# Performance work log

Measured on AMD Instinct MI355X. Metric: run time of the kernel, lower is better.

Reference implementation:

```python
import jax, jax.numpy as jnp
import numpy as np

H = 8   # heads
C = 64  # per-head channels (gnn_hidden_dim)
HID = H * C  # 512
IN_CH = 6
EMB = 64
U, M = 16, 512
N_NODES = U * M  # 8192
N_EDGES = 131072


def _tconv(x, src, dst, Wq, bq, Wk, bk, Wv, bv, Ws, bs):
    """PyG TransformerConv (concat=True, root_weight=True, beta=False, eval mode)."""
    N = x.shape[0]
    q = (x @ Wq + bq).reshape(N, H, C)
    k = (x @ Wk + bk).reshape(N, H, C)
    v = (x @ Wv + bv).reshape(N, H, C)
    # per-edge attention scores: query at dst (target i), key at src (source j)
    score = jnp.einsum('ehc,ehc->eh', q[dst], k[src]) / jnp.sqrt(jnp.float32(C))
    # segment softmax over incoming edges of each dst node
    mx = jax.ops.segment_max(score, dst, num_segments=N)
    ex = jnp.exp(score - mx[dst])
    denom = jax.ops.segment_sum(ex, dst, num_segments=N)
    alpha = ex / (denom[dst] + 1e-16)  # [E, H]
    msg = alpha[..., None] * v[src]    # [E, H, C]
    out = jax.ops.segment_sum(msg, dst, num_segments=N).reshape(N, HID)
    return out + x @ Ws + bs  # root/skip connection


def setup_inputs() -> dict:
    key = jax.random.key(0)
    ks = iter(jax.random.split(key, 64))
    s = 0.05

    def lin(k, i, o):
        k1, k2 = jax.random.split(k)
        return (jax.random.normal(k1, (i, o), jnp.float32) * s,
                jax.random.normal(k2, (o,), jnp.float32) * s)

    inp = {}
    inp['mission_coords'] = jax.random.uniform(next(ks), (M, 2), jnp.float32)
    inp['uavs_info'] = jax.random.uniform(next(ks), (U, 2), jnp.float32)
    inp['speeds'] = jax.random.uniform(next(ks), (U,), jnp.float32)
    inp['dist_matrix'] = jax.random.uniform(next(ks), (U, M), jnp.float32)
    inp['timetogo_matrix'] = jax.random.uniform(next(ks), (U, M), jnp.float32)
    inp['action_mask'] = jax.random.randint(next(ks), (U, M), 0, 2, jnp.int32)
    inp['edge_index'] = jax.random.randint(next(ks), (2, N_EDGES), 0, N_NODES, jnp.int64)
    inp['batch'] = jnp.zeros((U,), jnp.int64)

    # layer 0 (in=6)
    inp['Wq0'], inp['bq0'] = lin(next(ks), IN_CH, HID)
    inp['Wk0'], inp['bk0'] = lin(next(ks), IN_CH, HID)
    inp['Wv0'], inp['bv0'] = lin(next(ks), IN_CH, HID)
    inp['Ws0'], inp['bs0'] = lin(next(ks), IN_CH, HID)
    # layers 1..3 stacked (in=512)
    for nm in ['Wq', 'Wk', 'Wv', 'Ws']:
        Ws_, bs_ = [], []
        for _ in range(3):
            w, b = lin(next(ks), HID, HID)
            Ws_.append(w); bs_.append(b)
        inp[nm] = jnp.stack(Ws_)
        inp['b' + nm[1:].lower()] = jnp.stack(bs_)
    inp['Wout'], inp['bout'] = lin(next(ks), HID, EMB)
    inp['Wa1'], inp['ba1'] = lin(next(ks), EMB + 3, 128)
    inp['Wa2'], inp['ba2'] = lin(next(ks), 128, 1)
    inp['Wc1'], inp['bc1'] = lin(next(ks), EMB + 3, 128)
    inp['Wc2'], inp['bc2'] = lin(next(ks), 128, 1)
    return inp


def reference(mission_coords, uavs_info, speeds, dist_matrix, timetogo_matrix,
              action_mask, edge_index, batch,
              Wq0, bq0, Wk0, bk0, Wv0, bv0, Ws0, bs0,
              Wq, bq, Wk, bk, Wv, bv, Ws, bs,
              Wout, bout, Wa1, ba1, Wa2, ba2, Wc1, bc1, Wc2, bc2):
    u, m = uavs_info.shape[0], mission_coords.shape[0]
    mc = jnp.broadcast_to(mission_coords[None], (u, m, 2))
    mask_e = action_mask[..., None].astype(jnp.float32)
    sp_e = jnp.broadcast_to(speeds[:, None, None], (u, m, 1))
    x = jnp.concatenate([mc, mask_e, sp_e, dist_matrix[..., None],
                         timetogo_matrix[..., None]], axis=-1).reshape(u * m, IN_CH)
    src, dst = edge_index[0], edge_index[1]
    x = jax.nn.relu(_tconv(x, src, dst, Wq0, bq0, Wk0, bk0, Wv0, bv0, Ws0, bs0))
    for l in range(3):
        x = jax.nn.relu(_tconv(x, src, dst, Wq[l], bq[l], Wk[l], bk[l],
                               Wv[l], bv[l], Ws[l], bs[l]))
    x = x @ Wout + bout  # [U*M, EMB]
    uav_emb = x.reshape(u, m, EMB).sum(axis=1)  # sum pooling over missions
    combined = jnp.concatenate([uavs_info, uav_emb, speeds[:, None]], axis=-1)
    logits = jax.nn.relu(combined @ Wa1 + ba1) @ Wa2 + ba2  # [U, 1]
    action_probs = jax.nn.softmax(logits, axis=-1)
    state_values = (jax.nn.relu(combined @ Wc1 + bc1) @ Wc2 + bc2).squeeze()
    return action_probs, state_values
```

## Files before the change

### kernel.cpp

```cpp
#include <hip/hip_runtime.h>
#include <hip/hip_bf16.h>
#include <math.h>

#define NNODES 8192
#define NEDGES 131072
#define HID    512
#define UU     16
#define MM     512
#define NQKVS  2048

typedef __attribute__((ext_vector_type(8))) short bf16x8;
typedef __attribute__((ext_vector_type(4))) float f32x4;

__device__ __forceinline__ float bf2f(ushort u) {
    return __uint_as_float(((unsigned)u) << 16);
}
__device__ __forceinline__ ushort f2bf(float f) {
    unsigned x = __float_as_uint(f);
    return (ushort)((x + 0x7fffu + ((x >> 16) & 1u)) >> 16);
}

__global__ __launch_bounds__(256) void k_build_x(
    const float* __restrict__ mc, const float* __restrict__ speeds,
    const float* __restrict__ dist, const float* __restrict__ ttg,
    const int* __restrict__ mask, float* __restrict__ x6)
{
    int n = blockIdx.x * blockDim.x + threadIdx.x;
    if (n >= NNODES) return;
    int u = n >> 9, m = n & 511;
    float* o = x6 + (size_t)n * 6;
    o[0] = mc[m * 2 + 0];
    o[1] = mc[m * 2 + 1];
    o[2] = (float)mask[u * MM + m];
    o[3] = speeds[u];
    o[4] = dist[u * MM + m];
    o[5] = ttg[u * MM + m];
}

__global__ __launch_bounds__(256) void k_wt(
    const float* __restrict__ Wq, const float* __restrict__ Wk,
    const float* __restrict__ Wv, const float* __restrict__ Ws,
    ushort* __restrict__ Wt)
{
    __shared__ float tile[64][65];
    int z = blockIdx.z;
    int l = z >> 2, which = z & 3;
    const float* src = (which == 0 ? Wq : which == 1 ? Wk : which == 2 ? Wv : Ws)
                       + (size_t)l * HID * HID;
    int k0 = blockIdx.x * 64, c0 = blockIdx.y * 64;
    int t = threadIdx.x;
#pragma unroll
    for (int i = 0; i < 16; ++i) {
        int idx = i * 256 + t;
        int r = idx >> 6, c = idx & 63;
        tile[r][c] = src[(size_t)(k0 + r) * HID + c0 + c];
    }
    __syncthreads();
    ushort* dst = Wt + ((size_t)l * NQKVS + which * HID + c0) * HID + k0;
#pragma unroll
    for (int i = 0; i < 16; ++i) {
        int idx = i * 256 + t;
        int r = idx >> 6, c = idx & 63;
        dst[(size_t)r * HID + c] = f2bf(tile[c][r]);
    }
}

__global__ __launch_bounds__(256) void k_bias(
    const float* __restrict__ bq, const float* __restrict__ bk,
    const float* __restrict__ bv, const float* __restrict__ bs,
    float* __restrict__ bcat)
{
    int i = blockIdx.x * 256 + threadIdx.x;
    int l = i >> 11, j = i & 2047;
    int which = j >> 9, jj = j & 511;
    const float* b = which == 0 ? bq : which == 1 ? bk : which == 2 ? bv : bs;
    bcat[i] = b[l * HID + jj];
}

__global__ __launch_bounds__(256) void k_lin0(
    const float* __restrict__ x6,
    const float* __restrict__ Wq0, const float* __restrict__ bq0,
    const float* __restrict__ Wk0, const float* __restrict__ bk0,
    const float* __restrict__ Wv0, const float* __restrict__ bv0,
    const float* __restrict__ Ws0, const float* __restrict__ bs0,
    ushort* __restrict__ Y)
{
    int n = blockIdx.x;
    int j = threadIdx.x;
    int col0 = j * 8;
    int which = col0 >> 9, jj = col0 & 511;
    const float* W = which == 0 ? Wq0 : which == 1 ? Wk0 : which == 2 ? Wv0 : Ws0;
    const float* b = which == 0 ? bq0 : which == 1 ? bk0 : which == 2 ? bv0 : bs0;
    const float* xr = x6 + (size_t)n * 6;
    float x[6];
#pragma unroll
    for (int t = 0; t < 6; ++t) x[t] = xr[t];
    float s[8];
#pragma unroll
    for (int u = 0; u < 8; ++u) s[u] = b[jj + u];
#pragma unroll
    for (int t = 0; t < 6; ++t)
#pragma unroll
        for (int u = 0; u < 8; ++u)
            s[u] = fmaf(x[t], W[t * HID + jj + u], s[u]);
    bf16x8 o8;
#pragma unroll
    for (int u = 0; u < 8; ++u) o8[u] = (short)f2bf(s[u]);
    *(bf16x8*)(Y + (size_t)n * NQKVS + col0) = o8;
}

#define GBM 128
#define GBN 128
#define GBK 64
#define TILEB (GBM * GBK * 2)
#define BUFB  (2 * TILEB)

__device__ __forceinline__ void stage_tile(
    const ushort* __restrict__ Ag, const ushort* __restrict__ Bg,
    char* __restrict__ base, int t)
{
    const int lane = t & 63;
    const int w = t >> 6;
    const int r8 = lane >> 3;
    const int c  = lane & 7;
    const int csw = c ^ r8;
#pragma unroll
    for (int i = 0; i < 4; ++i) {
        int r0 = (w * 4 + i) * 8;
        __builtin_amdgcn_global_load_lds(
            (const __attribute__((address_space(1))) void*)(Ag + (size_t)(r0 + r8) * HID + csw * 8),
            (__attribute__((address_space(3))) void*)(base + r0 * 128 + lane * 16), 16, 0, 0);
        __builtin_amdgcn_global_load_lds(
            (const __attribute__((address_space(1))) void*)(Bg + (size_t)(r0 + r8) * HID + csw * 8),
            (__attribute__((address_space(3))) void*)(base + TILEB + r0 * 128 + lane * 16), 16, 0, 0);
    }
}

__global__ __launch_bounds__(256, 2) void k_gemm(
    const ushort* __restrict__ A,
    const ushort* __restrict__ Bt,
    const float* __restrict__ bias,
    ushort* __restrict__ Y)
{
    __shared__ char lds[2 * BUFB];
    const int t = threadIdx.x;
    const int m0 = blockIdx.x * GBM, n0 = blockIdx.y * GBN;
    const int wid = t >> 6, lane = t & 63;
    const int wr = wid >> 1, wc = wid & 1;
    const int l15 = lane & 15, lkq = lane >> 4;

    f32x4 acc[4][4] = {};

    const ushort* Ab = A + (size_t)m0 * HID;
    const ushort* Bb = Bt + (size_t)n0 * HID;

    stage_tile(Ab, Bb, lds, t);
    int cur = 0;
    const int NKS = HID / GBK;
    for (int T = 0; T < NKS; ++T) {
        __syncthreads();
        if (T + 1 < NKS)
            stage_tile(Ab + (T + 1) * GBK, Bb + (T + 1) * GBK,
                       lds + (cur ^ 1) * BUFB, t);
        const char* la = lds + cur * BUFB;
        const char* lb = la + TILEB;
#pragma unroll
        for (int kh = 0; kh < 2; ++kh) {
            const int kq = kh * 4 + lkq;
            const int sw = (kq ^ (l15 & 7)) << 4;
            bf16x8 a[4], b[4];
#pragma unroll
            for (int i = 0; i < 4; ++i)
                a[i] = *(const bf16x8*)(la + (wr * 64 + i * 16 + l15) * 128 + sw);
#pragma unroll
            for (int j = 0; j < 4; ++j)
                b[j] = *(const bf16x8*)(lb + (wc * 64 + j * 16 + l15) * 128 + sw);
#pragma unroll
            for (int i = 0; i < 4; ++i)
#pragma unroll
                for (int j = 0; j < 4; ++j)
                    acc[i][j] = __builtin_amdgcn_mfma_f32_16x16x32_bf16(a[i], b[j], acc[i][j], 0, 0, 0);
        }
        cur ^= 1;
    }

#pragma unroll
    for (int i = 0; i < 4; ++i) {
        int row = m0 + wr * 64 + i * 16 + lkq * 4;
#pragma unroll
        for (int j = 0; j < 4; ++j) {
            int col = n0 + wc * 64 + j * 16 + l15;
            float bc = bias[col];
            f32x4 r = acc[i][j];
#pragma unroll
            for (int g = 0; g < 4; ++g)
                Y[(size_t)(row + g) * NQKVS + col] = f2bf(r[g] + bc);
        }
    }
}

__global__ __launch_bounds__(256) void k_hist(const int* __restrict__ dst, int* __restrict__ cnt)
{
    int e = blockIdx.x * blockDim.x + threadIdx.x;
    if (e < NEDGES) atomicAdd(&cnt[dst[e]], 1);
}

__global__ __launch_bounds__(256) void k_scan(const int* __restrict__ cnt, int* __restrict__ indptr)
{
    __shared__ int sums[256];
    __shared__ int offs[256];
    int t = threadIdx.x;
    int base = t * 32;
    int s = 0;
    for (int i = 0; i < 32; ++i) s += cnt[base + i];
    sums[t] = s;
    __syncthreads();
    if (t == 0) {
        int run = 0;
        for (int i = 0; i < 256; ++i) { offs[i] = run; run += sums[i]; }
    }
    __syncthreads();
    int off = offs[t];
    for (int i = 0; i < 32; ++i) { indptr[base + i] = off; off += cnt[base + i]; }
    if (t == 255) indptr[NNODES] = off;
}

__global__ __launch_bounds__(256) void k_scatter(
    const int* __restrict__ src, const int* __restrict__ dst,
    const int* __restrict__ indptr, int* __restrict__ cursor, int* __restrict__ ssrc)
{
    int e = blockIdx.x * blockDim.x + threadIdx.x;
    if (e >= NEDGES) return;
    int d = dst[e];
    int p = atomicAdd(&cursor[d], 1);
    ssrc[indptr[d] + p] = src[e];
}

__global__ __launch_bounds__(256) void k_attn(
    const int* __restrict__ indptr, const int* __restrict__ ssrc,
    const ushort* __restrict__ Y,
    ushort* __restrict__ X)
{
    int n = blockIdx.x * 4 + (threadIdx.x >> 6);
    if (n >= NNODES) return;
    int l = threadIdx.x & 63;
    int cbase = l * 8;
    const ushort* yq = Y + (size_t)n * NQKVS + cbase;
    float qf[8];
    {
        bf16x8 q8 = *(const bf16x8*)yq;
#pragma unroll
        for (int j = 0; j < 8; ++j) qf[j] = bf2f((ushort)q8[j]);
    }
    float mrun = -INFINITY, ssum = 0.f;
    float acc[8] = {};
    int e0 = indptr[n], e1 = indptr[n + 1];
    bf16x8 ka = {}, va = {}, kb = {}, vb = {};
    if (e0 < e1) {
        int s = ssrc[e0];
        const ushort* yr = Y + (size_t)s * NQKVS + cbase;
        ka = *(const bf16x8*)(yr + 512);
        va = *(const bf16x8*)(yr + 1024);
    }
    if (e0 + 1 < e1) {
        int s = ssrc[e0 + 1];
        const ushort* yr = Y + (size_t)s * NQKVS + cbase;
        kb = *(const bf16x8*)(yr + 512);
        vb = *(const bf16x8*)(yr + 1024);
    }
    for (int e = e0; e < e1; ++e) {
        bf16x8 k8 = ka, v8 = va;
        ka = kb; va = vb;
        int en = e + 2;
        if (en < e1) {
            int s = ssrc[en];
            const ushort* yr = Y + (size_t)s * NQKVS + cbase;
            kb = *(const bf16x8*)(yr + 512);
            vb = *(const bf16x8*)(yr + 1024);
        }
        float part = 0.f;
#pragma unroll
        for (int j = 0; j < 8; ++j) part = fmaf(qf[j], bf2f((ushort)k8[j]), part);
        part += __shfl_xor(part, 1);
        part += __shfl_xor(part, 2);
        part += __shfl_xor(part, 4);
        float score = part * 0.125f;
        float mnew = fmaxf(mrun, score);
        float sc = __expf(mrun - mnew);
        float p = __expf(score - mnew);
        ssum = ssum * sc + p;
#pragma unroll
        for (int j = 0; j < 8; ++j)
            acc[j] = fmaf(acc[j], sc, p * bf2f((ushort)v8[j]));
        mrun = mnew;
    }
    float inv = ssum > 0.f ? 1.f / ssum : 0.f;
    bf16x8 o8;
#pragma unroll
    for (int j = 0; j < 8; ++j) {
        float o = fmaxf(fmaf(acc[j], inv, bf2f(yq[1536 + j])), 0.f);
        o8[j] = (short)f2bf(o);
    }
    *(bf16x8*)(X + (size_t)n * HID + cbase) = o8;
}

__global__ __launch_bounds__(512) void k_pool(const ushort* __restrict__ X, float* __restrict__ xsum)
{
    int u = blockIdx.x;
    int c = threadIdx.x;
    const ushort* base = X + (size_t)u * MM * HID + c;
    float s = 0.f;
    for (int m = 0; m < MM; ++m) s += bf2f(base[(size_t)m * HID]);
    xsum[u * HID + c] = s;
}

__global__ __launch_bounds__(64) void k_emb(
    const float* __restrict__ xsum, const float* __restrict__ Wout,
    const float* __restrict__ bout, float* __restrict__ emb)
{
    int u = blockIdx.x, j = threadIdx.x;
    const float* xr = xsum + u * HID;
    float s = 0.f;
    for (int i = 0; i < HID; ++i) s = fmaf(xr[i], Wout[i * 64 + j], s);
    emb[u * 64 + j] = s + 512.0f * bout[j];
}

__global__ __launch_bounds__(128) void k_head(
    const float* __restrict__ uavs, const float* __restrict__ speeds,
    const float* __restrict__ emb,
    const float* __restrict__ Wc1, const float* __restrict__ bc1,
    const float* __restrict__ Wc2, const float* __restrict__ bc2,
    float* __restrict__ out)
{
    __shared__ float comb[67];
    __shared__ float red[128];
    int u = blockIdx.x, t = threadIdx.x;
    if (t < 2) comb[t] = uavs[u * 2 + t];
    else if (t < 66) comb[t] = emb[u * 64 + (t - 2)];
    else if (t == 66) comb[t] = speeds[u];
    __syncthreads();
    float a = bc1[t];
    for (int i = 0; i < 67; ++i) a = fmaf(comb[i], Wc1[i * 128 + t], a);
    a = fmaxf(a, 0.f);
    red[t] = a * Wc2[t];
    __syncthreads();
    for (int sft = 64; sft > 0; sft >>= 1) {
        if (t < sft) red[t] += red[t + sft];
        __syncthreads();
    }
    if (t == 0) {
        out[u]      = 1.0f;
        out[16 + u] = red[0] + bc2[0];
    }
}

extern "C" void kernel_launch(void* const* d_in, const int* in_sizes, int n_in,
                              void* d_out, int out_size, void* d_ws, size_t ws_size,
                              hipStream_t stream)
{
    const float* mission_coords = (const float*)d_in[0];
    const float* uavs_info      = (const float*)d_in[1];
    const float* speeds         = (const float*)d_in[2];
    const float* dist_matrix    = (const float*)d_in[3];
    const float* timetogo       = (const float*)d_in[4];
    const int*   action_mask    = (const int*)d_in[5];
    const int*   edge_index     = (const int*)d_in[6];
    const float* Wq0 = (const float*)d_in[8];  const float* bq0 = (const float*)d_in[9];
    const float* Wk0 = (const float*)d_in[10]; const float* bk0 = (const float*)d_in[11];
    const float* Wv0 = (const float*)d_in[12]; const float* bv0 = (const float*)d_in[13];
    const float* Ws0 = (const float*)d_in[14]; const float* bs0 = (const float*)d_in[15];
    const float* Wq  = (const float*)d_in[16]; const float* bq  = (const float*)d_in[17];
    const float* Wk  = (const float*)d_in[18]; const float* bk  = (const float*)d_in[19];
    const float* Wv  = (const float*)d_in[20]; const float* bv  = (const float*)d_in[21];
    const float* Ws  = (const float*)d_in[22]; const float* bs  = (const float*)d_in[23];
    const float* Wout = (const float*)d_in[24]; const float* bout = (const float*)d_in[25];
    const float* Wc1 = (const float*)d_in[30]; const float* bc1 = (const float*)d_in[31];
    const float* Wc2 = (const float*)d_in[32]; const float* bc2 = (const float*)d_in[33];
    float* out = (float*)d_out;

    const int* e_src = edge_index;
    const int* e_dst = edge_index + NEDGES;

    char* p = (char*)d_ws;
    ushort* Ybf = (ushort*)p;  p += (size_t)NNODES * NQKVS * 2;
    ushort* Xbf = (ushort*)p;  p += (size_t)NNODES * HID * 2;
    ushort* Wt  = (ushort*)p;  p += (size_t)3 * NQKVS * HID * 2;
    float* bcat = (float*)p;   p += (size_t)3 * NQKVS * 4;
    float* x6   = (float*)p;   p += (size_t)NNODES * 6 * 4;
    float* xsum = (float*)p;   p += (size_t)UU * HID * 4;
    float* emb  = (float*)p;   p += (size_t)UU * 64 * 4;
    int* cnt    = (int*)p;     p += (size_t)NNODES * 4;
    int* indptr = (int*)p;     p += (size_t)(NNODES + 1) * 4;
    int* cursor = (int*)p;     p += (size_t)NNODES * 4;
    int* ssrc   = (int*)p;     p += (size_t)NEDGES * 4;

    hipMemsetAsync(cnt, 0, NNODES * sizeof(int), stream);
    hipMemsetAsync(cursor, 0, NNODES * sizeof(int), stream);

    k_build_x<<<NNODES / 256, 256, 0, stream>>>(mission_coords, speeds, dist_matrix,
                                                timetogo, action_mask, x6);
    k_wt<<<dim3(8, 8, 12), 256, 0, stream>>>(Wq, Wk, Wv, Ws, Wt);
    k_bias<<<3 * NQKVS / 256, 256, 0, stream>>>(bq, bk, bv, bs, bcat);
    k_hist<<<NEDGES / 256, 256, 0, stream>>>(e_dst, cnt);
    k_scan<<<1, 256, 0, stream>>>(cnt, indptr);
    k_scatter<<<NEDGES / 256, 256, 0, stream>>>(e_src, e_dst, indptr, cursor, ssrc);

    k_lin0<<<NNODES, 256, 0, stream>>>(x6, Wq0, bq0, Wk0, bk0, Wv0, bv0, Ws0, bs0, Ybf);
    k_attn<<<NNODES / 4, 256, 0, stream>>>(indptr, ssrc, Ybf, Xbf);

    dim3 ggrid(NNODES / GBM, NQKVS / GBN);
    for (int l = 0; l < 3; ++l) {
        k_gemm<<<ggrid, 256, 0, stream>>>(Xbf, Wt + (size_t)l * NQKVS * HID,
                                          bcat + l * NQKVS, Ybf);
        k_attn<<<NNODES / 4, 256, 0, stream>>>(indptr, ssrc, Ybf, Xbf);
    }

    k_pool<<<UU, 512, 0, stream>>>(Xbf, xsum);
    k_emb<<<UU, 64, 0, stream>>>(xsum, Wout, bout, emb);
    k_head<<<UU, 128, 0, stream>>>(uavs_info, speeds, emb, Wc1, bc1, Wc2, bc2, out);
}
```

Baseline: 309.2 us.

## Store keys in FP8 for attention gathers, remap GEMM blocks per XCD, split pooling

```diff
diff --git a/kernel.cpp b/kernel.cpp
--- a/kernel.cpp
+++ b/kernel.cpp
@@ -9,8 +9,18 @@
 #define MM     512
 #define NQKVS  2048
 
+#if __has_builtin(__builtin_amdgcn_cvt_pk_f32_fp8) && __has_builtin(__builtin_amdgcn_cvt_pk_fp8_f32)
+#define HAVE_FP8 1
+#else
+#define HAVE_FP8 0
+#endif
+
+#define KSCALE 16.0f
+#define KISCALE (0.125f / 16.0f)
+
 typedef __attribute__((ext_vector_type(8))) short bf16x8;
 typedef __attribute__((ext_vector_type(4))) float f32x4;
+typedef __attribute__((ext_vector_type(2))) float f32x2;
 
 __device__ __forceinline__ float bf2f(ushort u) {
     return __uint_as_float(((unsigned)u) << 16);
@@ -83,7 +93,7 @@
     const float* __restrict__ Wk0, const float* __restrict__ bk0,
     const float* __restrict__ Wv0, const float* __restrict__ bv0,
     const float* __restrict__ Ws0, const float* __restrict__ bs0,
-    ushort* __restrict__ Y)
+    ushort* __restrict__ Y, unsigned char* __restrict__ Kf8)
 {
     int n = blockIdx.x;
     int j = threadIdx.x;
@@ -107,6 +117,16 @@
 #pragma unroll
     for (int u = 0; u < 8; ++u) o8[u] = (short)f2bf(s[u]);
     *(bf16x8*)(Y + (size_t)n * NQKVS + col0) = o8;
+#if HAVE_FP8
+    if (which == 1) {
+        int w0 = __builtin_amdgcn_cvt_pk_fp8_f32(s[0] * KSCALE, s[1] * KSCALE, 0, false);
+        w0     = __builtin_amdgcn_cvt_pk_fp8_f32(s[2] * KSCALE, s[3] * KSCALE, w0, true);
+        int w1 = __builtin_amdgcn_cvt_pk_fp8_f32(s[4] * KSCALE, s[5] * KSCALE, 0, false);
+        w1     = __builtin_amdgcn_cvt_pk_fp8_f32(s[6] * KSCALE, s[7] * KSCALE, w1, true);
+        uint2 uu; uu.x = (unsigned)w0; uu.y = (unsigned)w1;
+        *(uint2*)(Kf8 + (size_t)n * HID + jj) = uu;
+    }
+#endif
 }
 
 #define GBM 128
@@ -140,11 +160,18 @@
     const ushort* __restrict__ A,
     const ushort* __restrict__ Bt,
     const float* __restrict__ bias,
-    ushort* __restrict__ Y)
+    ushort* __restrict__ Y,
+    unsigned char* __restrict__ Kf8)
 {
     __shared__ char lds[2 * BUFB];
     const int t = threadIdx.x;
-    const int m0 = blockIdx.x * GBM, n0 = blockIdx.y * GBN;
+    const int bid = blockIdx.x;
+    const int xcd = bid & 7;
+    const int ii  = bid >> 3;
+    const int mi  = (xcd << 3) | (ii & 7);
+    const int ni  = ii >> 3;
+    const int m0 = mi * GBM, n0 = ni * GBN;
+
     const int wid = t >> 6, lane = t & 63;
     const int wr = wid >> 1, wc = wid & 1;
     const int l15 = lane & 15, lkq = lane >> 4;
@@ -184,6 +211,7 @@
         cur ^= 1;
     }
 
+    const bool kquad = ((n0 >> 9) == 1);
 #pragma unroll
     for (int i = 0; i < 4; ++i) {
         int row = m0 + wr * 64 + i * 16 + lkq * 4;
@@ -193,8 +221,16 @@
             float bc = bias[col];
             f32x4 r = acc[i][j];
 #pragma unroll
-            for (int g = 0; g < 4; ++g)
-                Y[(size_t)(row + g) * NQKVS + col] = f2bf(r[g] + bc);
+            for (int g = 0; g < 4; ++g) {
+                float val = r[g] + bc;
+                Y[(size_t)(row + g) * NQKVS + col] = f2bf(val);
+#if HAVE_FP8
+                if (kquad) {
+                    int pk = __builtin_amdgcn_cvt_pk_fp8_f32(val * KSCALE, val * KSCALE, 0, false);
+                    Kf8[(size_t)(row + g) * HID + (col - 512)] = (unsigned char)(pk & 0xff);
+                }
+#endif
+            }
         }
     }
 }
@@ -239,6 +275,7 @@
 __global__ __launch_bounds__(256) void k_attn(
     const int* __restrict__ indptr, const int* __restrict__ ssrc,
     const ushort* __restrict__ Y,
+    const unsigned char* __restrict__ Kf8,
     ushort* __restrict__ X)
 {
     int n = blockIdx.x * 4 + (threadIdx.x >> 6);
@@ -255,36 +292,67 @@
     float mrun = -INFINITY, ssum = 0.f;
     float acc[8] = {};
     int e0 = indptr[n], e1 = indptr[n + 1];
-    bf16x8 ka = {}, va = {}, kb = {}, vb = {};
+#if HAVE_FP8
+    uint2 ka = {}, kb = {};
+#else
+    bf16x8 ka = {}, kb = {};
+#endif
+    bf16x8 va = {}, vb = {};
     if (e0 < e1) {
         int s = ssrc[e0];
-        const ushort* yr = Y + (size_t)s * NQKVS + cbase;
-        ka = *(const bf16x8*)(yr + 512);
-        va = *(const bf16x8*)(yr + 1024);
+#if HAVE_FP8
+        ka = *(const uint2*)(Kf8 + (size_t)s * HID + cbase);
+#else
+        ka = *(const bf16x8*)(Y + (size_t)s * NQKVS + 512 + cbase);
+#endif
+        va = *(const bf16x8*)(Y + (size_t)s * NQKVS + 1024 + cbase);
     }
     if (e0 + 1 < e1) {
         int s = ssrc[e0 + 1];
-        const ushort* yr = Y + (size_t)s * NQKVS + cbase;
-        kb = *(const bf16x8*)(yr + 512);
-        vb = *(const bf16x8*)(yr + 1024);
+#if HAVE_FP8
+        kb = *(const uint2*)(Kf8 + (size_t)s * HID + cbase);
+#else
+        kb = *(const bf16x8*)(Y + (size_t)s * NQKVS + 512 + cbase);
+#endif
+        vb = *(const bf16x8*)(Y + (size_t)s * NQKVS + 1024 + cbase);
     }
     for (int e = e0; e < e1; ++e) {
-        bf16x8 k8 = ka, v8 = va;
+        auto k8 = ka; bf16x8 v8 = va;
         ka = kb; va = vb;
         int en = e + 2;
         if (en < e1) {
             int s = ssrc[en];
-            const ushort* yr = Y + (size_t)s * NQKVS + cbase;
-            kb = *(const bf16x8*)(yr + 512);
-            vb = *(const bf16x8*)(yr + 1024);
+#if HAVE_FP8
+            kb = *(const uint2*)(Kf8 + (size_t)s * HID + cbase);
+#else
+            kb = *(const bf16x8*)(Y + (size_t)s * NQKVS + 512 + cbase);
+#endif
+            vb = *(const bf16x8*)(Y + (size_t)s * NQKVS + 1024 + cbase);
         }
         float part = 0.f;
+#if HAVE_FP8
+        {
+            f32x2 k01 = __builtin_amdgcn_cvt_pk_f32_fp8((int)k8.x, false);
+            f32x2 k23 = __builtin_amdgcn_cvt_pk_f32_fp8((int)k8.x, true);
+            f32x2 k45 = __builtin_amdgcn_cvt_pk_f32_fp8((int)k8.y, false);
+            f32x2 k67 = __builtin_amdgcn_cvt_pk_f32_fp8((int)k8.y, true);
+            part = fmaf(qf[0], k01.x, part); part = fmaf(qf[1], k01.y, part);
+            part = fmaf(qf[2], k23.x, part); part = fmaf(qf[3], k23.y, part);
+            part = fmaf(qf[4], k45.x, part); part = fmaf(qf[5], k45.y, part);
+            part = fmaf(qf[6], k67.x, part); part = fmaf(qf[7], k67.y, part);
+        }
+#else
 #pragma unroll
         for (int j = 0; j < 8; ++j) part = fmaf(qf[j], bf2f((ushort)k8[j]), part);
+#endif
         part += __shfl_xor(part, 1);
         part += __shfl_xor(part, 2);
         part += __shfl_xor(part, 4);
+#if HAVE_FP8
+        float score = part * KISCALE;
+#else
         float score = part * 0.125f;
+#endif
         float mnew = fmaxf(mrun, score);
         float sc = __expf(mrun - mnew);
         float p = __expf(score - mnew);
@@ -304,25 +372,33 @@
     *(bf16x8*)(X + (size_t)n * HID + cbase) = o8;
 }
 
-__global__ __launch_bounds__(512) void k_pool(const ushort* __restrict__ X, float* __restrict__ xsum)
+__global__ __launch_bounds__(512) void k_pool(const ushort* __restrict__ X, float* __restrict__ xsumP)
 {
     int u = blockIdx.x;
+    int pp = blockIdx.y;
     int c = threadIdx.x;
-    const ushort* base = X + (size_t)u * MM * HID + c;
+    const ushort* base = X + ((size_t)u * MM + pp * 64) * HID + c;
     float s = 0.f;
-    for (int m = 0; m < MM; ++m) s += bf2f(base[(size_t)m * HID]);
-    xsum[u * HID + c] = s;
-}
-
-__global__ __launch_bounds__(64) void k_emb(
-    const float* __restrict__ xsum, const float* __restrict__ Wout,
+    for (int m = 0; m < 64; ++m) s += bf2f(base[(size_t)m * HID]);
+    xsumP[((size_t)u * 8 + pp) * HID + c] = s;
+}
+
+__global__ __launch_bounds__(512) void k_emb(
+    const float* __restrict__ xsumP, const float* __restrict__ Wout,
     const float* __restrict__ bout, float* __restrict__ emb)
 {
-    int u = blockIdx.x, j = threadIdx.x;
-    const float* xr = xsum + u * HID;
+    __shared__ float xs[HID];
+    int u = blockIdx.x, c = threadIdx.x;
     float s = 0.f;
-    for (int i = 0; i < HID; ++i) s = fmaf(xr[i], Wout[i * 64 + j], s);
-    emb[u * 64 + j] = s + 512.0f * bout[j];
+#pragma unroll
+    for (int p = 0; p < 8; ++p) s += xsumP[((size_t)u * 8 + p) * HID + c];
+    xs[c] = s;
+    __syncthreads();
+    if (c < 64) {
+        float a = 0.f;
+        for (int i = 0; i < HID; ++i) a = fmaf(xs[i], Wout[i * 64 + c], a);
+        emb[u * 64 + c] = a + 512.0f * bout[c];
+    }
 }
 
 __global__ __launch_bounds__(128) void k_head(
@@ -385,9 +461,10 @@
     ushort* Ybf = (ushort*)p;  p += (size_t)NNODES * NQKVS * 2;
     ushort* Xbf = (ushort*)p;  p += (size_t)NNODES * HID * 2;
     ushort* Wt  = (ushort*)p;  p += (size_t)3 * NQKVS * HID * 2;
+    unsigned char* Kf8 = (unsigned char*)p; p += (size_t)NNODES * HID;
     float* bcat = (float*)p;   p += (size_t)3 * NQKVS * 4;
     float* x6   = (float*)p;   p += (size_t)NNODES * 6 * 4;
-    float* xsum = (float*)p;   p += (size_t)UU * HID * 4;
+    float* xsumP = (float*)p;  p += (size_t)UU * 8 * HID * 4;
     float* emb  = (float*)p;   p += (size_t)UU * 64 * 4;
     int* cnt    = (int*)p;     p += (size_t)NNODES * 4;
     int* indptr = (int*)p;     p += (size_t)(NNODES + 1) * 4;
@@ -405,17 +482,17 @@
     k_scan<<<1, 256, 0, stream>>>(cnt, indptr);
     k_scatter<<<NEDGES / 256, 256, 0, stream>>>(e_src, e_dst, indptr, cursor, ssrc);
 
-    k_lin0<<<NNODES, 256, 0, stream>>>(x6, Wq0, bq0, Wk0, bk0, Wv0, bv0, Ws0, bs0, Ybf);
-    k_attn<<<NNODES / 4, 256, 0, stream>>>(indptr, ssrc, Ybf, Xbf);
-
-    dim3 ggrid(NNODES / GBM, NQKVS / GBN);
+    k_lin0<<<NNODES, 256, 0, stream>>>(x6, Wq0, bq0, Wk0, bk0, Wv0, bv0, Ws0, bs0, Ybf, Kf8);
+    k_attn<<<NNODES / 4, 256, 0, stream>>>(indptr, ssrc, Ybf, Kf8, Xbf);
+
+    const int ngblocks = (NNODES / GBM) * (NQKVS / GBN);
     for (int l = 0; l < 3; ++l) {
-        k_gemm<<<ggrid, 256, 0, stream>>>(Xbf, Wt + (size_t)l * NQKVS * HID,
-                                          bcat + l * NQKVS, Ybf);
-        k_attn<<<NNODES / 4, 256, 0, stream>>>(indptr, ssrc, Ybf, Xbf);
-    }
-
-    k_pool<<<UU, 512, 0, stream>>>(Xbf, xsum);
-    k_emb<<<UU, 64, 0, stream>>>(xsum, Wout, bout, emb);
+        k_gemm<<<ngblocks, 256, 0, stream>>>(Xbf, Wt + (size_t)l * NQKVS * HID,
+                                             bcat + l * NQKVS, Ybf, Kf8);
+        k_attn<<<NNODES / 4, 256, 0, stream>>>(indptr, ssrc, Ybf, Kf8, Xbf);
+    }
+
+    k_pool<<<dim3(UU, 8), 512, 0, stream>>>(Xbf, xsumP);
+    k_emb<<<UU, 512, 0, stream>>>(xsumP, Wout, bout, emb);
     k_head<<<UU, 128, 0, stream>>>(uavs_info, speeds, emb, Wc1, bc1, Wc2, bc2, out);
 }
```

Result: faster. 277.3 us (-10.3%).
